# Optimization experiments

Hardware: AMD Instinct MI355X
Metric: run time of the kernel (lower is better)

Reference implementation:

```python
import math
import jax, jax.numpy as jnp
import numpy as np

N_HEADS = 8
EPS = 1e-6


def setup_inputs() -> dict:
    key = jax.random.key(0)
    k0, k1, k2, k3, k4 = jax.random.split(key, 5)
    B, T, E = 2, 1024, 512
    s = 1.0 / math.sqrt(E)
    x = jax.random.normal(k0, (B, T, E), dtype=jnp.float32)
    w_qkv = jax.random.normal(k1, (3 * E, E), dtype=jnp.float32) * s
    b_qkv = jax.random.normal(k2, (3 * E,), dtype=jnp.float32) * s
    w_out = jax.random.normal(k3, (E, E), dtype=jnp.float32) * s
    b_out = jax.random.normal(k4, (E,), dtype=jnp.float32) * s
    return {"x": x, "w_qkv": w_qkv, "b_qkv": b_qkv, "w_out": w_out, "b_out": b_out}


def reference(x, w_qkv, b_qkv, w_out, b_out):
    B, T, C = x.shape
    H = N_HEADS
    d = C // H

    qkv = x @ w_qkv.T + b_qkv                      # [B,T,3C]
    q, k, v = jnp.split(qkv, 3, axis=-1)

    def to_heads(t):
        return t.reshape(B, T, H, d).transpose(0, 2, 1, 3).astype(jnp.float32)  # [B,H,T,d]

    q, k, v = to_heads(q), to_heads(k), to_heads(v)

    pos = jnp.arange(T, dtype=jnp.float32)
    ang = (math.pi / 2) * pos / T
    cos_w = jnp.cos(ang)[None, None, :, None]      # [1,1,T,1]
    sin_w = jnp.sin(ang)[None, None, :, None]

    q_prime = jax.nn.relu(q)
    k_prime = jax.nn.relu(k)
    q_cos, q_sin = q_prime * cos_w, q_prime * sin_w
    k_cos, k_sin = k_prime * cos_w, k_prime * sin_w

    # causal linear attention via cumulative outer products (cosFormer)
    kv_cos_cs = jnp.cumsum(jnp.einsum('bhtd,bhte->bhtde', k_cos, v), axis=2)
    context = jnp.einsum('bhtd,bhtde->bhte', q_cos, kv_cos_cs)
    kv_sin_cs = jnp.cumsum(jnp.einsum('bhtd,bhte->bhtde', k_sin, v), axis=2)
    context = context + jnp.einsum('bhtd,bhtde->bhte', q_sin, kv_sin_cs)

    norm = (jnp.einsum('bhtd,bhtd->bht', q_cos, jnp.cumsum(k_cos, axis=2))
            + jnp.einsum('bhtd,bhtd->bht', q_sin, jnp.cumsum(k_sin, axis=2)))
    out = context / (norm[..., None] + EPS)        # [B,H,T,d]

    out = out.astype(x.dtype).transpose(0, 2, 1, 3).reshape(B, T, C)
    return out @ w_out.T + b_out
```

## Files before the change

kernel.cpp:

```cpp
#include <hip/hip_runtime.h>

typedef __bf16 bf16_t;
typedef __bf16 bf16x4 __attribute__((ext_vector_type(4)));
typedef __bf16 bf16x8 __attribute__((ext_vector_type(8)));
typedef float f32x4 __attribute__((ext_vector_type(4)));

#define T_SEQ 1024
#define EMB   512
#define NH    8
#define HD    64
#define BATCH 2
#define NBH   (BATCH*NH)
#define CHUNK 64
#define NCHUNK (T_SEQ/CHUNK)
#define NBLK  (NBH*NCHUNK)
#define LDA   72
#define LDK   68


__global__ __launch_bounds__(256) void cvt3_kernel(
    const float* __restrict__ x, const float* __restrict__ wq,
    const float* __restrict__ wo,
    bf16_t* __restrict__ xb, bf16_t* __restrict__ wqb, bf16_t* __restrict__ wob)
{
    int i = blockIdx.x * 256 + threadIdx.x;
    const float* s; bf16_t* d; int off;
    if (i < 262144)      { s = x;  d = xb;  off = i; }
    else if (i < 458752) { s = wq; d = wqb; off = i - 262144; }
    else                 { s = wo; d = wob; off = i - 458752; }
    float4 v = ((const float4*)s)[off];
    bf16x4 o;
    o[0] = (bf16_t)v.x; o[1] = (bf16_t)v.y;
    o[2] = (bf16_t)v.z; o[3] = (bf16_t)v.w;
    ((bf16x4*)d)[off] = o;
}

__global__ __launch_bounds__(256) void qkv_sum_kernel(
    const bf16_t* __restrict__ X, const bf16_t* __restrict__ W,
    const float* __restrict__ bias,
    bf16_t* __restrict__ qq, bf16_t* __restrict__ kk, bf16_t* __restrict__ vv,
    bf16_t* __restrict__ Ssc, bf16_t* __restrict__ Sss,
    float* __restrict__ zc, float* __restrict__ zs)
{
    __shared__ __align__(16) bf16_t sk[CHUNK * LDK];
    __shared__ __align__(16) bf16_t sv[CHUNK * LDK];
    __shared__ float cwt[CHUNK], swt[CHUNK];

    const int m0 = blockIdx.x * 64;
    const int h  = blockIdx.y;
    const int b  = m0 >> 10;
    const int ch = (m0 & 1023) >> 6;
    const int blk = (b * NH + h) * NCHUNK + ch;

    if (threadIdx.x < CHUNK) {
        int tg = ch * CHUNK + threadIdx.x;
        float ang = 1.5707963267948966f * (float)tg * (1.0f / (float)T_SEQ);
        cwt[threadIdx.x] = cosf(ang);
        swt[threadIdx.x] = sinf(ang);
    }

    const int w = threadIdx.x >> 6;
    const int lane = threadIdx.x & 63;
    if (w < 3) {
        const int rsel = lane & 15;
        const int koff = (lane >> 4) * 8;
        const int n0 = w * 512 + h * 64;
        f32x4 acc[4][4] = {};
        const bf16_t* Ap = X + (m0 + rsel) * EMB + koff;
        const bf16_t* Bp = W + (n0 + rsel) * EMB + koff;
#pragma unroll 4
        for (int k0 = 0; k0 < EMB; k0 += 32) {
            bf16x8 af[4], bfr[4];
            for (int i = 0; i < 4; ++i)
                af[i] = *(const bf16x8*)(Ap + i * 16 * EMB + k0);
            for (int j = 0; j < 4; ++j)
                bfr[j] = *(const bf16x8*)(Bp + j * 16 * EMB + k0);
            for (int i = 0; i < 4; ++i)
                for (int j = 0; j < 4; ++j)
                    acc[i][j] = __builtin_amdgcn_mfma_f32_16x16x32_bf16(
                        af[i], bfr[j], acc[i][j], 0, 0, 0);
        }
        for (int j = 0; j < 4; ++j) {
            const int feat = j * 16 + rsel;
            const float bn = bias[n0 + feat];
            for (int i = 0; i < 4; ++i) {
                const int tl0 = i * 16 + (lane >> 4) * 4;
                for (int r = 0; r < 4; ++r) {
                    const int tl = tl0 + r;
                    const int t = (m0 & 1023) + tl;
                    float val = acc[i][j][r] + bn;
                    int di = ((b * NH + h) * T_SEQ + t) * HD + feat;
                    if (w == 0) {
                        qq[di] = (bf16_t)fmaxf(val, 0.f);
                    } else if (w == 1) {
                        bf16_t kb = (bf16_t)fmaxf(val, 0.f);
                        kk[di] = kb;
                        sk[tl * LDK + feat] = kb;
                    } else {
                        bf16_t vb = (bf16_t)val;
                        vv[di] = vb;
                        sv[tl * LDK + feat] = vb;
                    }
                }
            }
        }
    }
    __syncthreads();

    const int i  = threadIdx.x & 63;
    const int jg = (threadIdx.x >> 6) * 16;
    float ac[16], as[16];
    for (int jj = 0; jj < 16; ++jj) { ac[jj] = 0.f; as[jj] = 0.f; }
    float zca = 0.f, zsa = 0.f;
    const bool zown = (jg == 0);
    for (int t = 0; t < CHUNK; ++t) {
        float kv = (float)sk[t * LDK + i];
        float kc_ = kv * cwt[t];
        float ks_ = kv * swt[t];
        if (zown) { zca += kc_; zsa += ks_; }
        for (int jj = 0; jj < 16; ++jj) {
            float vj = (float)sv[t * LDK + jg + jj];
            ac[jj] += kc_ * vj;
            as[jj] += ks_ * vj;
        }
    }
    bf16_t* oc = Ssc + blk * HD * HD;
    bf16_t* os = Sss + blk * HD * HD;
    for (int jj = 0; jj < 16; ++jj) {
        oc[(jg + jj) * HD + i] = (bf16_t)ac[jj];
        os[(jg + jj) * HD + i] = (bf16_t)as[jj];
    }
    if (zown) {
        zc[blk * HD + i] = zca;
        zs[blk * HD + i] = zsa;
    }
}

__global__ __launch_bounds__(256) void chunk_out_kernel(
    const bf16_t* __restrict__ qq, const bf16_t* __restrict__ kk,
    const bf16_t* __restrict__ vv,
    const bf16_t* __restrict__ SscT, const bf16_t* __restrict__ SssT,
    const float* __restrict__ zc, const float* __restrict__ zs,
    bf16_t* __restrict__ Y)
{
    const int blk = blockIdx.x;
    const int bh = blk >> 4, ch = blk & 15;
    __shared__ __align__(16) bf16_t sq [CHUNK * LDA];
    __shared__ __align__(16) bf16_t sk [CHUNK * LDA];
    __shared__ __align__(16) bf16_t svT[CHUNK * LDA];
    __shared__ __align__(16) bf16_t sct[CHUNK * LDA];
    __shared__ __align__(16) bf16_t sst[CHUNK * LDA];
    __shared__ __align__(16) bf16_t sp [CHUNK * LDA];
    __shared__ float cwt[CHUNK], swt[CHUNK], cosd[CHUNK];
    __shared__ float zcl[CHUNK], zsl[CHUNK], nrm[CHUNK];

    const int base = blk * CHUNK * HD;
    for (int i = threadIdx.x; i < CHUNK * HD / 8; i += 256) {
        int row = i >> 3, g = i & 7;
        ((uint4*)(sq + row * LDA))[g]  = ((const uint4*)(qq + base))[i];
        ((uint4*)(sk + row * LDA))[g]  = ((const uint4*)(kk + base))[i];
        bf16x8 v8 = *(const bf16x8*)(vv + base + i * 8);
        int t = i >> 3, bb = i & 7;
        int tg8 = t >> 3, tf = t & 7;
        for (int j = 0; j < 8; ++j) {
            int e = bb * 8 + j;
            int pg = (tg8 + bb) & 7;
            svT[e * LDA + pg * 8 + tf] = v8[j];
        }
    }
    {
        const int e0 = threadIdx.x * 16;
        float accC[16], accS[16];
        for (int j = 0; j < 16; ++j) { accC[j] = 0.f; accS[j] = 0.f; }
        const int sb = bh * NCHUNK * HD * HD + e0;
#pragma unroll 2
        for (int c = 0; c < ch; ++c) {
            const bf16x8* pc = (const bf16x8*)(SscT + sb + c * HD * HD);
            const bf16x8* ps = (const bf16x8*)(SssT + sb + c * HD * HD);
            bf16x8 c0 = pc[0], c1 = pc[1], s0 = ps[0], s1 = ps[1];
            for (int j = 0; j < 8; ++j) {
                accC[j] += (float)c0[j];  accC[8 + j] += (float)c1[j];
                accS[j] += (float)s0[j];  accS[8 + j] += (float)s1[j];
            }
        }
        const int row = threadIdx.x >> 2, col = (threadIdx.x & 3) * 16;
        bf16x8 oc0, oc1, os0, os1;
        for (int j = 0; j < 8; ++j) {
            oc0[j] = (bf16_t)accC[j];  oc1[j] = (bf16_t)accC[8 + j];
            os0[j] = (bf16_t)accS[j];  os1[j] = (bf16_t)accS[8 + j];
        }
        *(bf16x8*)(sct + row * LDA + col) = oc0;
        *(bf16x8*)(sct + row * LDA + col + 8) = oc1;
        *(bf16x8*)(sst + row * LDA + col) = os0;
        *(bf16x8*)(sst + row * LDA + col + 8) = os1;
    }
    if (threadIdx.x < HD) {
        int tl = threadIdx.x;
        float s = 0.f;
        for (int c = 0; c < ch; ++c) s += zc[(bh * NCHUNK + c) * HD + tl];
        zcl[tl] = s;
        int tg = ch * CHUNK + tl;
        float angg = 1.5707963267948966f * (float)tg * (1.0f / (float)T_SEQ);
        cwt[tl] = cosf(angg);
        swt[tl] = sinf(angg);
        cosd[tl] = cosf(1.5707963267948966f * (float)tl * (1.0f / (float)T_SEQ));
    } else if (threadIdx.x < 2 * HD) {
        int i = threadIdx.x - HD;
        float s = 0.f;
        for (int c = 0; c < ch; ++c) s += zs[(bh * NCHUNK + c) * HD + i];
        zsl[i] = s;
    }
    __syncthreads();

    const int w = threadIdx.x >> 6;
    const int lane = threadIdx.x & 63;
    const int rsel = lane & 15;
    const int koff = (lane >> 4) * 8;
    const int myrow = w * 16 + rsel;

    bf16x8 aq0 = *(const bf16x8*)(sq + myrow * LDA + koff);
    bf16x8 aq1 = *(const bf16x8*)(sq + myrow * LDA + koff + 32);
    for (int nt = 0; nt < 4; ++nt) {
        const int n0 = nt * 16;
        f32x4 pacc = {0.f, 0.f, 0.f, 0.f};
        bf16x8 b0 = *(const bf16x8*)(sk + (n0 + rsel) * LDA + koff);
        bf16x8 b1 = *(const bf16x8*)(sk + (n0 + rsel) * LDA + koff + 32);
        pacc = __builtin_amdgcn_mfma_f32_16x16x32_bf16(aq0, b0, pacc, 0, 0, 0);
        pacc = __builtin_amdgcn_mfma_f32_16x16x32_bf16(aq1, b1, pacc, 0, 0, 0);
        const int s = n0 + (lane & 15);
        const int tb = w * 16 + (lane >> 4) * 4;
        for (int r = 0; r < 4; ++r) {
            int t = tb + r;
            float p = (s <= t) ? pacc[r] * cosd[t - s] : 0.f;
            sp[t * LDA + s] = (bf16_t)p;
        }
    }

    if (lane < 16) {
        int row = w * 16 + lane;
        float nv = 0.f;
        const bf16x8* pr = (const bf16x8*)(sp + row * LDA);
        for (int g = 0; g < 8; ++g) {
            bf16x8 pv = pr[g];
            for (int j = 0; j < 8; ++j) nv += (float)pv[j];
        }
        float cwr = cwt[row], swr = swt[row];
        const bf16x8* qr = (const bf16x8*)(sq + row * LDA);
        for (int g = 0; g < 8; ++g) {
            bf16x8 qv = qr[g];
            for (int j = 0; j < 8; ++j)
                nv += (float)qv[j] * (cwr * zcl[g * 8 + j] + swr * zsl[g * 8 + j]);
        }
        nrm[row] = nv;
    }

    const float cwq = cwt[myrow], swq = swt[myrow];
    bf16x8 qc0, qc1, qs0, qs1;
    for (int j = 0; j < 8; ++j) {
        qc0[j] = (bf16_t)((float)aq0[j] * cwq);
        qc1[j] = (bf16_t)((float)aq1[j] * cwq);
        qs0[j] = (bf16_t)((float)aq0[j] * swq);
        qs1[j] = (bf16_t)((float)aq1[j] * swq);
    }
    bf16x8 ap0 = *(const bf16x8*)(sp + myrow * LDA + koff);
    bf16x8 ap1 = *(const bf16x8*)(sp + myrow * LDA + koff + 32);

    const int b = bh >> 3, h = bh & 7;
    const int g0 = koff >> 3;
    for (int nt = 0; nt < 4; ++nt) {
        const int n0 = nt * 16;
        const int ee = n0 + rsel;
        const int rot = (ee >> 3) & 7;
        const bf16_t* bvp0 = svT + ee * LDA + (((g0 + rot) & 7) << 3);
        const bf16_t* bvp1 = svT + ee * LDA + (((g0 + 4 + rot) & 7) << 3);
        const bf16_t* bcp = sct + ee * LDA + koff;
        const bf16_t* bsp = sst + ee * LDA + koff;
        f32x4 acc = {0.f, 0.f, 0.f, 0.f};
        acc = __builtin_amdgcn_mfma_f32_16x16x32_bf16(ap0, *(const bf16x8*)(bvp0), acc, 0, 0, 0);
        acc = __builtin_amdgcn_mfma_f32_16x16x32_bf16(ap1, *(const bf16x8*)(bvp1), acc, 0, 0, 0);
        acc = __builtin_amdgcn_mfma_f32_16x16x32_bf16(qc0, *(const bf16x8*)(bcp), acc, 0, 0, 0);
        acc = __builtin_amdgcn_mfma_f32_16x16x32_bf16(qc1, *(const bf16x8*)(bcp + 32), acc, 0, 0, 0);
        acc = __builtin_amdgcn_mfma_f32_16x16x32_bf16(qs0, *(const bf16x8*)(bsp), acc, 0, 0, 0);
        acc = __builtin_amdgcn_mfma_f32_16x16x32_bf16(qs1, *(const bf16x8*)(bsp + 32), acc, 0, 0, 0);
        const int col = n0 + (lane & 15);
        const int tb = w * 16 + (lane >> 4) * 4;
        for (int r = 0; r < 4; ++r) {
            int row = tb + r;
            float inv = 1.0f / (nrm[row] + 1e-6f);
            int tg = ch * CHUNK + row;
            Y[((b * T_SEQ + tg) * EMB) + h * HD + col] = (bf16_t)(acc[r] * inv);
        }
    }
}

__global__ __launch_bounds__(256) void out_gemm_kernel(
    const bf16_t* __restrict__ Yb, const bf16_t* __restrict__ W,
    const float* __restrict__ bias, float* __restrict__ out)
{
    const int w = threadIdx.x >> 6;
    const int lane = threadIdx.x & 63;
    const int rsel = lane & 15;
    const int koff = (lane >> 4) * 8;
    const int m0 = blockIdx.x * 64 + (w & 1) * 32;
    const int n0 = blockIdx.y * 64 + (w >> 1) * 32;
    f32x4 acc[2][2] = {};
    const bf16_t* Ap = Yb + (m0 + rsel) * EMB + koff;
    const bf16_t* Bp = W + (n0 + rsel) * EMB + koff;
#pragma unroll 8
    for (int k0 = 0; k0 < EMB; k0 += 32) {
        bf16x8 af[2], bfr[2];
        for (int i = 0; i < 2; ++i)
            af[i] = *(const bf16x8*)(Ap + i * 16 * EMB + k0);
        for (int j = 0; j < 2; ++j)
            bfr[j] = *(const bf16x8*)(Bp + j * 16 * EMB + k0);
        for (int i = 0; i < 2; ++i)
            for (int j = 0; j < 2; ++j)
                acc[i][j] = __builtin_amdgcn_mfma_f32_16x16x32_bf16(
                    af[i], bfr[j], acc[i][j], 0, 0, 0);
    }
    for (int j = 0; j < 2; ++j) {
        const int n = n0 + j * 16 + rsel;
        const float bn = bias[n];
        for (int i = 0; i < 2; ++i) {
            const int mb = m0 + i * 16 + (lane >> 4) * 4;
            for (int r = 0; r < 4; ++r)
                out[(mb + r) * EMB + n] = acc[i][j][r] + bn;
        }
    }
}

extern "C" void kernel_launch(void* const* d_in, const int* in_sizes, int n_in,
                              void* d_out, int out_size, void* d_ws, size_t ws_size,
                              hipStream_t stream) {
    const float* x     = (const float*)d_in[0];
    const float* w_qkv = (const float*)d_in[1];
    const float* b_qkv = (const float*)d_in[2];
    const float* w_out = (const float*)d_in[3];
    const float* b_out = (const float*)d_in[4];
    float* out = (float*)d_out;

    char* w = (char*)d_ws;
    const size_t N_X   = (size_t)BATCH * T_SEQ * EMB;
    const size_t N_WQ  = (size_t)3 * EMB * EMB;
    const size_t N_WO  = (size_t)EMB * EMB;
    bf16_t* xb   = (bf16_t*)w;                 w += N_X  * sizeof(bf16_t);
    bf16_t* wqb  = (bf16_t*)w;                 w += N_WQ * sizeof(bf16_t);
    bf16_t* wob  = (bf16_t*)w;                 w += N_WO * sizeof(bf16_t);
    const size_t SZ_BHTD = (size_t)NBH * T_SEQ * HD * sizeof(bf16_t);
    bf16_t* qq = (bf16_t*)w;                   w += SZ_BHTD;
    bf16_t* kk = (bf16_t*)w;                   w += SZ_BHTD;
    bf16_t* vv = (bf16_t*)w;                   w += SZ_BHTD;
    bf16_t* Y  = (bf16_t*)w;                   w += SZ_BHTD;
    bf16_t* SscT = (bf16_t*)w;                 w += (size_t)NBLK * HD * HD * sizeof(bf16_t);
    bf16_t* SssT = (bf16_t*)w;                 w += (size_t)NBLK * HD * HD * sizeof(bf16_t);
    float* zc = (float*)w;                     w += (size_t)NBLK * HD * sizeof(float);
    float* zs = (float*)w;

    cvt3_kernel<<<2048, 256, 0, stream>>>(x, w_qkv, w_out, xb, wqb, wob);
    qkv_sum_kernel<<<dim3(32, 8), 256, 0, stream>>>(
        xb, wqb, b_qkv, qq, kk, vv, SscT, SssT, zc, zs);
    chunk_out_kernel<<<NBLK, 256, 0, stream>>>(qq, kk, vv, SscT, SssT, zc, zs, Y);
    out_gemm_kernel<<<dim3(2048 / 64, 512 / 64), 256, 0, stream>>>(
        Y, wob, b_out, out);
}
```

Before: 118.8 us.

## Split QKV GEMM K-dimension across two waves per output with LDS reduction

Doubles the qkv_sum block to 512 threads. Each of Q/K/V now gets two waves that each cover half of the 512-wide K dimension, and the partial sums are reduced through new float LDS buffers. The chunk-state accumulation is spread over 8 waves with 8 columns each instead of 4 waves with 16. The goal is to halve the serial MFMA and global-load chain per wave in this 256-block launch, which is under-occupied. The cost is extra LDS (about 35KB more), extra barriers, and a serialized Q reduction phase.

```diff
diff --git a/kernel.cpp b/kernel.cpp
--- a/kernel.cpp
+++ b/kernel.cpp
@@ -35,7 +35,7 @@
     ((bf16x4*)d)[off] = o;
 }
 
-__global__ __launch_bounds__(256) void qkv_sum_kernel(
+__global__ __launch_bounds__(512) void qkv_sum_kernel(
     const bf16_t* __restrict__ X, const bf16_t* __restrict__ W,
     const float* __restrict__ bias,
     bf16_t* __restrict__ qq, bf16_t* __restrict__ kk, bf16_t* __restrict__ vv,
@@ -44,6 +44,8 @@
 {
     __shared__ __align__(16) bf16_t sk[CHUNK * LDK];
     __shared__ __align__(16) bf16_t sv[CHUNK * LDK];
+    __shared__ __align__(16) float  Pa[CHUNK * LDK];
+    __shared__ __align__(16) float  Pb[CHUNK * LDK];
     __shared__ float cwt[CHUNK], swt[CHUNK];
 
     const int m0 = blockIdx.x * 64;
@@ -59,17 +61,22 @@
         swt[threadIdx.x] = sinf(ang);
     }
 
-    const int w = threadIdx.x >> 6;
+    const int ww   = threadIdx.x >> 6;
     const int lane = threadIdx.x & 63;
-    if (w < 3) {
-        const int rsel = lane & 15;
-        const int koff = (lane >> 4) * 8;
-        const int n0 = w * 512 + h * 64;
-        f32x4 acc[4][4] = {};
-        const bf16_t* Ap = X + (m0 + rsel) * EMB + koff;
-        const bf16_t* Bp = W + (n0 + rsel) * EMB + koff;
+    const int sel  = ww & 3;
+    const int kh   = ww >> 2;
+    const int rsel = lane & 15;
+    const int koff = (lane >> 4) * 8;
+    const int tl0g = (lane >> 4) * 4;
+
+    f32x4 acc[4][4] = {};
+    if (sel < 3) {
+        const int n0 = sel * 512 + h * 64;
+        const int kb = kh * 256;
+        const bf16_t* Ap = X + (m0 + rsel) * EMB + kb + koff;
+        const bf16_t* Bp = W + (n0 + rsel) * EMB + kb + koff;
 #pragma unroll 4
-        for (int k0 = 0; k0 < EMB; k0 += 32) {
+        for (int k0 = 0; k0 < 256; k0 += 32) {
             bf16x8 af[4], bfr[4];
             for (int i = 0; i < 4; ++i)
                 af[i] = *(const bf16x8*)(Ap + i * 16 * EMB + k0);
@@ -80,22 +87,34 @@
                     acc[i][j] = __builtin_amdgcn_mfma_f32_16x16x32_bf16(
                         af[i], bfr[j], acc[i][j], 0, 0, 0);
         }
+    }
+
+    if (kh == 1 && (sel == 1 || sel == 2)) {
+        float* P = (sel == 2) ? Pa : Pb;
+        for (int j = 0; j < 4; ++j)
+            for (int i = 0; i < 4; ++i)
+                *(f32x4*)(P + (j * 16 + rsel) * LDK + i * 16 + tl0g) = acc[i][j];
+    }
+    __syncthreads();
+
+    if (kh == 0 && (sel == 1 || sel == 2)) {
+        const float* P = (sel == 2) ? Pa : Pb;
+        const int n0 = sel * 512 + h * 64;
         for (int j = 0; j < 4; ++j) {
             const int feat = j * 16 + rsel;
             const float bn = bias[n0 + feat];
             for (int i = 0; i < 4; ++i) {
-                const int tl0 = i * 16 + (lane >> 4) * 4;
+                const int tl0 = i * 16 + tl0g;
+                f32x4 p = *(const f32x4*)(P + feat * LDK + tl0);
                 for (int r = 0; r < 4; ++r) {
                     const int tl = tl0 + r;
                     const int t = (m0 & 1023) + tl;
-                    float val = acc[i][j][r] + bn;
+                    float val = acc[i][j][r] + p[r] + bn;
                     int di = ((b * NH + h) * T_SEQ + t) * HD + feat;
-                    if (w == 0) {
-                        qq[di] = (bf16_t)fmaxf(val, 0.f);
-                    } else if (w == 1) {
-                        bf16_t kb = (bf16_t)fmaxf(val, 0.f);
-                        kk[di] = kb;
-                        sk[tl * LDK + feat] = kb;
+                    if (sel == 1) {
+                        bf16_t kb2 = (bf16_t)fmaxf(val, 0.f);
+                        kk[di] = kb2;
+                        sk[tl * LDK + feat] = kb2;
                     } else {
                         bf16_t vb = (bf16_t)val;
                         vv[di] = vb;
@@ -107,10 +126,36 @@
     }
     __syncthreads();
 
-    const int i  = threadIdx.x & 63;
-    const int jg = (threadIdx.x >> 6) * 16;
-    float ac[16], as[16];
-    for (int jj = 0; jj < 16; ++jj) { ac[jj] = 0.f; as[jj] = 0.f; }
+    if (kh == 1 && sel == 0) {
+        for (int j = 0; j < 4; ++j)
+            for (int i = 0; i < 4; ++i)
+                *(f32x4*)(Pa + (j * 16 + rsel) * LDK + i * 16 + tl0g) = acc[i][j];
+    }
+    __syncthreads();
+
+    if (kh == 0 && sel == 0) {
+        const int n0 = h * 64;
+        for (int j = 0; j < 4; ++j) {
+            const int feat = j * 16 + rsel;
+            const float bn = bias[n0 + feat];
+            for (int i = 0; i < 4; ++i) {
+                const int tl0 = i * 16 + tl0g;
+                f32x4 p = *(const f32x4*)(Pa + feat * LDK + tl0);
+                for (int r = 0; r < 4; ++r) {
+                    const int tl = tl0 + r;
+                    const int t = (m0 & 1023) + tl;
+                    float val = acc[i][j][r] + p[r] + bn;
+                    int di = ((b * NH + h) * T_SEQ + t) * HD + feat;
+                    qq[di] = (bf16_t)fmaxf(val, 0.f);
+                }
+            }
+        }
+    }
+
+    const int i  = lane;
+    const int jg = ww * 8;
+    float ac[8], as[8];
+    for (int jj = 0; jj < 8; ++jj) { ac[jj] = 0.f; as[jj] = 0.f; }
     float zca = 0.f, zsa = 0.f;
     const bool zown = (jg == 0);
     for (int t = 0; t < CHUNK; ++t) {
@@ -118,7 +163,7 @@
         float kc_ = kv * cwt[t];
         float ks_ = kv * swt[t];
         if (zown) { zca += kc_; zsa += ks_; }
-        for (int jj = 0; jj < 16; ++jj) {
+        for (int jj = 0; jj < 8; ++jj) {
             float vj = (float)sv[t * LDK + jg + jj];
             ac[jj] += kc_ * vj;
             as[jj] += ks_ * vj;
@@ -126,7 +171,7 @@
     }
     bf16_t* oc = Ssc + blk * HD * HD;
     bf16_t* os = Sss + blk * HD * HD;
-    for (int jj = 0; jj < 16; ++jj) {
+    for (int jj = 0; jj < 8; ++jj) {
         oc[(jg + jj) * HD + i] = (bf16_t)ac[jj];
         os[(jg + jj) * HD + i] = (bf16_t)as[jj];
     }
@@ -357,7 +402,7 @@
     float* zs = (float*)w;
 
     cvt3_kernel<<<2048, 256, 0, stream>>>(x, w_qkv, w_out, xb, wqb, wob);
-    qkv_sum_kernel<<<dim3(32, 8), 256, 0, stream>>>(
+    qkv_sum_kernel<<<dim3(32, 8), 512, 0, stream>>>(
         xb, wqb, b_qkv, qq, kk, vv, SscT, SssT, zc, zs);
     chunk_out_kernel<<<NBLK, 256, 0, stream>>>(qq, kk, vv, SscT, SssT, zc, zs, Y);
     out_gemm_kernel<<<dim3(2048 / 64, 512 / 64), 256, 0, stream>>>(
```

Result: faster. 113.8 us (-4.2%).
